# Optimization experiments

Hardware: AMD Instinct MI355X
Metric: run time of the kernel (lower is better)

Reference implementation:

```python
import jax, jax.numpy as jnp
import numpy as np

B, S, H, V = 2, 2048, 1024, 32000
SDS = [64, 128, 256]
EPS = 1e-5


def _ln(x, g, b):
    m = jnp.mean(x, -1, keepdims=True)
    v = jnp.var(x, -1, keepdims=True)
    return (x - m) * jax.lax.rsqrt(v + EPS) * g + b


def _layer(x, A_log, Wb, Wc, D, Wg, bg, Wo, bo, g, be):
    # x: [B,S,H]; state dim N = A_log.shape[0]
    A = jnp.exp(A_log)
    gate = jax.nn.sigmoid(jnp.einsum('bsh,nh->bsn', x, Wg) + bg)
    Bx = jnp.einsum('bsh,nh->bsn', x, Wb)
    u = gate * Bx  # [B,S,N]

    def step(s, u_t):
        s = A * s + u_t
        return s, s

    s0 = jnp.zeros((x.shape[0], A.shape[0]), x.dtype)
    _, states = jax.lax.scan(step, s0, jnp.swapaxes(u, 0, 1))  # [S,B,N]
    states = jnp.swapaxes(states, 0, 1)
    y = jnp.einsum('bsn,hn->bsh', states, Wc) + D * x
    out = _ln(y + x, g, be)
    return out @ Wo.T + bo  # dropout is identity (p used in eval / p=0)


def setup_inputs() -> dict:
    key = jax.random.key(0)
    ks = iter(jax.random.split(key, 64))
    d = {}
    d['x'] = jax.random.randint(next(ks), (B, S), 0, V)
    d['E'] = jax.random.normal(next(ks), (V, H), jnp.float32) * 0.02
    for i, N in enumerate(SDS):
        d[f'A{i}'] = jnp.log(jnp.exp(jnp.full((N,), -0.5)) + 0.1 * jax.random.normal(next(ks), (N,)))
        d[f'Wb{i}'] = jax.random.normal(next(ks), (N, H), jnp.float32) * 0.02
        d[f'Wc{i}'] = jax.random.normal(next(ks), (H, N), jnp.float32) * 0.02
        d[f'D{i}'] = jax.random.normal(next(ks), (H,), jnp.float32)
        d[f'Wg{i}'] = jax.random.normal(next(ks), (N, H), jnp.float32) * 0.02
        d[f'bg{i}'] = jnp.zeros((N,), jnp.float32)
        d[f'Wo{i}'] = jax.random.normal(next(ks), (H, H), jnp.float32) * 0.02
        d[f'bo{i}'] = jnp.zeros((H,), jnp.float32)
        d[f'g{i}'] = jnp.ones((H,), jnp.float32)
        d[f'be{i}'] = jnp.zeros((H,), jnp.float32)
    d['Wf'] = jax.random.normal(next(ks), (H, 3 * H), jnp.float32) * 0.02
    d['bf'] = jnp.zeros((H,), jnp.float32)
    d['gf'] = jnp.ones((H,), jnp.float32)
    d['bef'] = jnp.zeros((H,), jnp.float32)
    d['Wh'] = jax.random.normal(next(ks), (V, H), jnp.float32) * 0.02
    d['bh'] = jnp.zeros((V,), jnp.float32)
    return d


def reference(x, E,
              A0, Wb0, Wc0, D0, Wg0, bg0, Wo0, bo0, g0, be0,
              A1, Wb1, Wc1, D1, Wg1, bg1, Wo1, bo1, g1, be1,
              A2, Wb2, Wc2, D2, Wg2, bg2, Wo2, bo2, g2, be2,
              Wf, bf, gf, bef, Wh, bh):
    emb = E[x]  # [B,S,H]
    o0 = _layer(emb, A0, Wb0, Wc0, D0, Wg0, bg0, Wo0, bo0, g0, be0)
    o1 = _layer(emb, A1, Wb1, Wc1, D1, Wg1, bg1, Wo1, bo1, g1, be1)
    o2 = _layer(emb, A2, Wb2, Wc2, D2, Wg2, bg2, Wo2, bo2, g2, be2)
    combined = jnp.concatenate([o0, o1, o2], axis=-1)  # [B,S,3H]
    fused = combined @ Wf.T + bf
    fused = _ln(fused + emb, gf, bef)
    logits = fused @ Wh.T + bh  # [B,S,V]
    return logits
```

## Files before the change

kernel.cpp:

```cpp
#include <hip/hip_runtime.h>
#include <hip/hip_bf16.h>

#define Hd 1024
#define Bdim 2
#define Sd 2048
#define BSd 4096
#define Vd 32000
#define EPSf 1e-5f
#define CH 16
#define NCH 128
#define NT3 448

typedef __attribute__((ext_vector_type(8))) short short8;
typedef __attribute__((ext_vector_type(4))) float f32x4;
typedef __attribute__((ext_vector_type(4))) unsigned short us4;

__device__ __forceinline__ unsigned short f2bf(float f) {
  union { float f; unsigned int u; } v; v.f = f;
  return (unsigned short)((v.u + 0x7fffu + ((v.u >> 16) & 1u)) >> 16);
}

typedef __attribute__((address_space(1))) const void gvoid_t;
typedef __attribute__((address_space(3))) void svoid_t;
__device__ __forceinline__ void gl_lds16(const void* g, void* s) {
  __builtin_amdgcn_global_load_lds((gvoid_t*)g, (svoid_t*)s, 16, 0, 0);
}

struct CvtTab {
  const float* src[11];
  unsigned short* dst[11];
  int start[12];
};
__global__ void k_cvt_all(CvtTab tab) {
  int b = blockIdx.x;
  int j = 0;
  while (j < 10 && b >= tab.start[j + 1]) ++j;
  size_t i = (size_t)(b - tab.start[j]) * 256 + threadIdx.x;
  f32x4 v = *(const f32x4*)(tab.src[j] + i * 4);
  us4 o;
  o[0] = f2bf(v[0]); o[1] = f2bf(v[1]); o[2] = f2bf(v[2]); o[3] = f2bf(v[3]);
  *(us4*)(tab.dst[j] + i * 4) = o;
}

__global__ void k_cvtT(const float* __restrict__ s0, const float* __restrict__ s1,
                       const float* __restrict__ s2, unsigned short* __restrict__ dst) {
  const float* src = blockIdx.z == 0 ? s0 : (blockIdx.z == 1 ? s1 : s2);
  unsigned short* d = dst + (size_t)blockIdx.z * Hd * Hd;
  __shared__ float tile[32][33];
  int tx = threadIdx.x & 31, ty = threadIdx.x >> 5;
  int bx = blockIdx.x * 32, by = blockIdx.y * 32;
  #pragma unroll
  for (int i = 0; i < 4; ++i)
    tile[ty + i * 8][tx] = src[(size_t)(by + ty + i * 8) * Hd + bx + tx];
  __syncthreads();
  #pragma unroll
  for (int i = 0; i < 4; ++i)
    d[(size_t)(bx + ty + i * 8) * Hd + by + tx] = f2bf(tile[tx][ty + i * 8]);
}

__global__ void k_biasf(const float* __restrict__ Wf_, const float* __restrict__ bfb,
                        const float* __restrict__ bo0, const float* __restrict__ bo1,
                        const float* __restrict__ bo2, float* __restrict__ biasf) {
  int h = blockIdx.x, t = threadIdx.x;
  float s = 0.f;
  for (int c = t; c < 3072; c += 256) {
    float b = c < 1024 ? bo0[c] : (c < 2048 ? bo1[c - 1024] : bo2[c - 2048]);
    s += Wf_[(size_t)h * 3072 + c] * b;
  }
  #pragma unroll
  for (int o = 32; o >= 1; o >>= 1) s += __shfl_xor(s, o);
  __shared__ float red[4];
  if ((t & 63) == 0) red[t >> 6] = s;
  __syncthreads();
  if (t == 0) biasf[h] = bfb[h] + red[0] + red[1] + red[2] + red[3];
}

__global__ void k_setup(const float* A0, const float* A1, const float* A2,
                        const float* b0, const float* b1, const float* b2,
                        const float* D0, const float* D1, const float* D2,
                        const float* g0, const float* g1, const float* g2,
                        const float* e0, const float* e1, const float* e2,
                        float* Alog448, float* bg448,
                        float* D3, float* g3, float* be3) {
  int t = blockIdx.x * 256 + threadIdx.x;
  if (t < NT3) {
    int l = t < 64 ? 0 : (t < 192 ? 1 : 2);
    int o = t - (l == 0 ? 0 : (l == 1 ? 64 : 192));
    Alog448[t] = (l == 0 ? A0 : (l == 1 ? A1 : A2))[o];
    bg448[t]   = (l == 0 ? b0 : (l == 1 ? b1 : b2))[o];
  }
  if (t < 3072) {
    int l = t >> 10, o = t & 1023;
    D3[t]  = (l == 0 ? D0 : (l == 1 ? D1 : D2))[o];
    g3[t]  = (l == 0 ? g0 : (l == 1 ? g1 : g2))[o];
    be3[t] = (l == 0 ? e0 : (l == 1 ? e1 : e2))[o];
  }
}

__global__ void k_embed(const int* __restrict__ x, const float* __restrict__ E,
                        float* __restrict__ emb, unsigned short* __restrict__ embbf) {
  int row = blockIdx.x, t = threadIdx.x;
  int id = x[row];
  f32x4 v = *(const f32x4*)(E + (size_t)id * Hd + t * 4);
  *(f32x4*)(emb + (size_t)row * Hd + t * 4) = v;
  us4 o;
  o[0] = f2bf(v[0]); o[1] = f2bf(v[1]); o[2] = f2bf(v[2]); o[3] = f2bf(v[3]);
  *(us4*)(embbf + (size_t)row * Hd + t * 4) = o;
}

template<int BM, int BN, int WM, int WN, int BF16_OUT>
__launch_bounds__(WM * WN * 64)
__global__ void gemm2ph(const unsigned short* __restrict__ A,
                        const unsigned short* __restrict__ Bw,
                        const float* __restrict__ bias,
                        void* __restrict__ Cv,
                        int N, int K, int lda, int ldb, int ldc, int coff, int tm)
{
  constexpr int NT = WM * WN * 64;
  constexpr int MF = BM / WM / 16;
  constexpr int NF = BN / WN / 16;
  constexpr int ASZ = BM * 64;
  constexpr int BSZ = BN * 64;
  constexpr int AR = (ASZ * 2) / (NT * 16);
  constexpr int BR = (BSZ * 2) / (NT * 16);
  __shared__ __align__(16) unsigned short Sm[2 * (ASZ + BSZ)];

  int T = gridDim.x;
  int orig = blockIdx.x;
  int q = T >> 3, r = T & 7;
  int xc = orig & 7, sdv = orig >> 3;
  int wgid = (xc < r ? xc * (q + 1) : r * (q + 1) + (xc - r) * q) + sdv;
  int n_t = wgid / tm, m_t = wgid % tm;
  int row0 = m_t * BM, col0 = n_t * BN;

  int tid = threadIdx.x;
  int wave = tid >> 6, lane = tid & 63;
  int wm = wave / WN, wn = wave % WN;
  int wr = wm * (BM / WM), wc = wn * (BN / WN);
  int lr = lane & 15;
  int klane = lane >> 4;

  f32x4 acc[MF][NF] = {};

  auto stage = [&](int buf, int k0) {
    unsigned short* Ab = Sm + buf * (ASZ + BSZ);
    unsigned short* Bb = Ab + ASZ;
    #pragma unroll
    for (int j = 0; j < AR; ++j) {
      int slot = j * NT + tid;
      int lrow = slot >> 3, c16 = slot & 7;
      int scol = (c16 ^ (lrow & 7)) * 8;
      gl_lds16(A + (size_t)(row0 + lrow) * lda + k0 + scol, Ab + (j * NT + wave * 64) * 8);
    }
    #pragma unroll
    for (int j = 0; j < BR; ++j) {
      int slot = j * NT + tid;
      int lrow = slot >> 3, c16 = slot & 7;
      int scol = (c16 ^ (lrow & 7)) * 8;
      int brow = col0 + lrow;
      if (brow >= N) brow = N - 1;
      gl_lds16(Bw + (size_t)brow * ldb + k0 + scol, Bb + (j * NT + wave * 64) * 8);
    }
  };

  auto compute = [&](int buf) {
    const unsigned short* Ab = Sm + buf * (ASZ + BSZ);
    const unsigned short* Bb = Ab + ASZ;
    #pragma unroll
    for (int kk = 0; kk < 2; ++kk) {
      short8 afr[MF], bfr[NF];
      #pragma unroll
      for (int m = 0; m < MF; ++m) {
        int row = wr + m * 16 + lr;
        int cs = (kk * 4 + klane) ^ (row & 7);
        afr[m] = *(const short8*)(Ab + row * 64 + cs * 8);
      }
      #pragma unroll
      for (int n = 0; n < NF; ++n) {
        int row = wc + n * 16 + lr;
        int cs = (kk * 4 + klane) ^ (row & 7);
        bfr[n] = *(const short8*)(Bb + row * 64 + cs * 8);
      }
      #pragma unroll
      for (int m = 0; m < MF; ++m)
        #pragma unroll
        for (int n = 0; n < NF; ++n)
          acc[m][n] = __builtin_amdgcn_mfma_f32_16x16x32_bf16(afr[m], bfr[n], acc[m][n], 0, 0, 0);
    }
  };

  int nt = K >> 6;
  stage(0, 0);
  __syncthreads();
  for (int t = 0; t < nt - 1; ++t) {
    stage((t & 1) ^ 1, (t + 1) * 64);
    compute(t & 1);
    __syncthreads();
  }
  compute((nt - 1) & 1);

  int rb = (lane >> 4) * 4;
  #pragma unroll
  for (int m = 0; m < MF; ++m) {
    #pragma unroll
    for (int n = 0; n < NF; ++n) {
      int gcol = col0 + wc + n * 16 + lr;
      if (gcol >= N) continue;
      float bv = bias ? bias[gcol] : 0.f;
      #pragma unroll
      for (int j = 0; j < 4; ++j) {
        int grow = row0 + wr + m * 16 + rb + j;
        float val = acc[m][n][j] + bv;
        if (BF16_OUT)
          ((unsigned short*)Cv)[(size_t)grow * ldc + coff + gcol] = f2bf(val);
        else
          ((float*)Cv)[(size_t)grow * ldc + coff + gcol] = val;
      }
    }
  }
}

__launch_bounds__(256)
__global__ void gemm_wc3(const unsigned short* __restrict__ St,
                         const unsigned short* __restrict__ Wc,
                         float* __restrict__ Cv)
{
  constexpr int ASZ = 128 * 64, BSZ = 128 * 64;
  __shared__ __align__(16) unsigned short Sm[2 * (ASZ + BSZ)];
  int T = gridDim.x;
  int orig = blockIdx.x;
  int q = T >> 3, r = T & 7;
  int xc = orig & 7, sdv = orig >> 3;
  int wgid = (xc < r ? xc * (q + 1) : r * (q + 1) + (xc - r) * q) + sdv;
  int l = wgid % 3;
  int w2 = wgid / 3;
  int n_t = w2 >> 5, m_t = w2 & 31;
  const int owgl = l == 0 ? 0 : (l == 1 ? 64 : 192);
  const int K = 64 << l;
  const unsigned short* A = St + owgl;
  const unsigned short* Bw = Wc + (size_t)owgl * Hd;
  int row0 = m_t * 128, col0 = n_t * 128;

  int tid = threadIdx.x;
  int wave = tid >> 6, lane = tid & 63;
  int wm = wave >> 1, wn = wave & 1;
  int wr = wm * 64, wc = wn * 64;
  int lr = lane & 15, klane = lane >> 4;

  f32x4 acc[4][4] = {};
  auto stage = [&](int buf, int k0) {
    unsigned short* Ab = Sm + buf * (ASZ + BSZ);
    unsigned short* Bb = Ab + ASZ;
    #pragma unroll
    for (int j = 0; j < 4; ++j) {
      int slot = j * 256 + tid;
      int lrow = slot >> 3, c16 = slot & 7;
      int scol = (c16 ^ (lrow & 7)) * 8;
      gl_lds16(A + (size_t)(row0 + lrow) * NT3 + k0 + scol, Ab + (j * 256 + wave * 64) * 8);
      gl_lds16(Bw + (size_t)(col0 + lrow) * K + k0 + scol, Bb + (j * 256 + wave * 64) * 8);
    }
  };
  auto compute = [&](int buf) {
    const unsigned short* Ab = Sm + buf * (ASZ + BSZ);
    const unsigned short* Bb = Ab + ASZ;
    #pragma unroll
    for (int kk = 0; kk < 2; ++kk) {
      short8 afr[4], bfr[4];
      #pragma unroll
      for (int m = 0; m < 4; ++m) {
        int row = wr + m * 16 + lr;
        int cs = (kk * 4 + klane) ^ (row & 7);
        afr[m] = *(const short8*)(Ab + row * 64 + cs * 8);
      }
      #pragma unroll
      for (int n = 0; n < 4; ++n) {
        int row = wc + n * 16 + lr;
        int cs = (kk * 4 + klane) ^ (row & 7);
        bfr[n] = *(const short8*)(Bb + row * 64 + cs * 8);
      }
      #pragma unroll
      for (int m = 0; m < 4; ++m)
        #pragma unroll
        for (int n = 0; n < 4; ++n)
          acc[m][n] = __builtin_amdgcn_mfma_f32_16x16x32_bf16(afr[m], bfr[n], acc[m][n], 0, 0, 0);
    }
  };
  int nt = K >> 6;
  stage(0, 0);
  __syncthreads();
  for (int t = 0; t < nt - 1; ++t) {
    stage((t & 1) ^ 1, (t + 1) * 64);
    compute(t & 1);
    __syncthreads();
  }
  compute((nt - 1) & 1);

  int rb = (lane >> 4) * 4;
  #pragma unroll
  for (int m = 0; m < 4; ++m)
    #pragma unroll
    for (int n = 0; n < 4; ++n) {
      int gcol = l * Hd + col0 + wc + n * 16 + lr;
      #pragma unroll
      for (int j = 0; j < 4; ++j) {
        int grow = row0 + wr + m * 16 + rb + j;
        Cv[(size_t)grow * 3072 + gcol] = acc[m][n][j];
      }
    }
}

__launch_bounds__(256)
__global__ void gemm_bd3(const unsigned short* __restrict__ Awf,
                         const unsigned short* __restrict__ Bwo,
                         unsigned short* __restrict__ Cw)
{
  constexpr int ASZ = 128 * 64, BSZ = 128 * 64;
  __shared__ __align__(16) unsigned short Sm[2 * (ASZ + BSZ)];
  int T = gridDim.x;
  int orig = blockIdx.x;
  int q = T >> 3, r = T & 7;
  int xc = orig & 7, sdv = orig >> 3;
  int wgid = (xc < r ? xc * (q + 1) : r * (q + 1) + (xc - r) * q) + sdv;
  int n_g = wgid / 8, m_t = wgid % 8;
  int li = n_g >> 3, n_t = n_g & 7;
  const unsigned short* A = Awf + li * Hd;
  const unsigned short* Bw = Bwo + ((size_t)li << 20);
  int row0 = m_t * 128, col0 = n_t * 128;

  int tid = threadIdx.x;
  int wave = tid >> 6, lane = tid & 63;
  int wm = wave >> 1, wn = wave & 1;
  int wr = wm * 64, wc = wn * 64;
  int lr = lane & 15, klane = lane >> 4;

  f32x4 acc[4][4] = {};
  auto stage = [&](int buf, int k0) {
    unsigned short* Ab = Sm + buf * (ASZ + BSZ);
    unsigned short* Bb = Ab + ASZ;
    #pragma unroll
    for (int j = 0; j < 4; ++j) {
      int slot = j * 256 + tid;
      int lrow = slot >> 3, c16 = slot & 7;
      int scol = (c16 ^ (lrow & 7)) * 8;
      gl_lds16(A + (size_t)(row0 + lrow) * 3072 + k0 + scol, Ab + (j * 256 + wave * 64) * 8);
      gl_lds16(Bw + (size_t)(col0 + lrow) * 1024 + k0 + scol, Bb + (j * 256 + wave * 64) * 8);
    }
  };
  auto compute = [&](int buf) {
    const unsigned short* Ab = Sm + buf * (ASZ + BSZ);
    const unsigned short* Bb = Ab + ASZ;
    #pragma unroll
    for (int kk = 0; kk < 2; ++kk) {
      short8 afr[4], bfr[4];
      #pragma unroll
      for (int m = 0; m < 4; ++m) {
        int row = wr + m * 16 + lr;
        int cs = (kk * 4 + klane) ^ (row & 7);
        afr[m] = *(const short8*)(Ab + row * 64 + cs * 8);
      }
      #pragma unroll
      for (int n = 0; n < 4; ++n) {
        int row = wc + n * 16 + lr;
        int cs = (kk * 4 + klane) ^ (row & 7);
        bfr[n] = *(const short8*)(Bb + row * 64 + cs * 8);
      }
      #pragma unroll
      for (int m = 0; m < 4; ++m)
        #pragma unroll
        for (int n = 0; n < 4; ++n)
          acc[m][n] = __builtin_amdgcn_mfma_f32_16x16x32_bf16(afr[m], bfr[n], acc[m][n], 0, 0, 0);
    }
  };
  stage(0, 0);
  __syncthreads();
  for (int t = 0; t < 15; ++t) {
    stage((t & 1) ^ 1, (t + 1) * 64);
    compute(t & 1);
    __syncthreads();
  }
  compute(1);

  int rb = (lane >> 4) * 4;
  #pragma unroll
  for (int m = 0; m < 4; ++m)
    #pragma unroll
    for (int n = 0; n < 4; ++n) {
      int gcol = li * Hd + col0 + wc + n * 16 + lr;
      #pragma unroll
      for (int j = 0; j < 4; ++j) {
        int grow = row0 + wr + m * 16 + rb + j;
        Cw[(size_t)grow * 3072 + gcol] = f2bf(acc[m][n][j]);
      }
    }
}

__launch_bounds__(512)
__global__ void gemm8ph(const unsigned short* __restrict__ A,
                        const unsigned short* __restrict__ Bw,
                        const float* __restrict__ bias,
                        float* __restrict__ Cv,
                        int N, int K, int lda, int ldb, int ldc, int tn)
{
  __shared__ __align__(16) unsigned short Sm[65536];

  int wgid = blockIdx.x;
  int grp = wgid >> 8;
  int rem = wgid & 255;
  int n_t = grp * 16 + (rem >> 4);
  int m_t = rem & 15;
  int row0 = m_t * 256, col0 = n_t * 256;

  int tid = threadIdx.x;
  int wave = tid >> 6, lane = tid & 63;
  int wm = wave >> 2, wn = wave & 3;
  int lr = lane & 15, klane = lane >> 4;

  f32x4 acc[8][4] = {};

  auto stageA = [&](int b, int h, int kt) {
    unsigned short* base = Sm + (b * 2 + h) * 8192;
    #pragma unroll
    for (int j = 0; j < 2; ++j) {
      int slot = j * 512 + tid;
      int lrow = slot >> 3, c16 = slot & 7;
      int scol = (c16 ^ (lrow & 7)) * 8;
      gl_lds16(A + (size_t)(row0 + h * 128 + lrow) * lda + kt * 64 + scol,
               base + (j * 512 + wave * 64) * 8);
    }
  };
  auto stageB = [&](int b, int h, int kt) {
    unsigned short* base = Sm + 32768 + (b * 2 + h) * 8192;
    #pragma unroll
    for (int j = 0; j < 2; ++j) {
      int slot = j * 512 + tid;
      int lrow = slot >> 3, c16 = slot & 7;
      int scol = (c16 ^ (lrow & 7)) * 8;
      gl_lds16(Bw + (size_t)(col0 + h * 128 + lrow) * ldb + kt * 64 + scol,
               base + (j * 512 + wave * 64) * 8);
    }
  };
  auto readA = [&](short8* afr, int b, int mh, int kk) {
    const unsigned short* base = Sm + (b * 2 + mh) * 8192;
    #pragma unroll
    for (int f = 0; f < 4; ++f) {
      int rowin = f * 32 + wm * 16 + lr;
      int cs = (kk * 4 + klane) ^ (rowin & 7);
      afr[f] = *(const short8*)(base + rowin * 64 + cs * 8);
    }
  };
  auto readB = [&](short8* bfr, int b, int kk) {
    #pragma unroll
    for (int n = 0; n < 4; ++n) {
      int rowin = (n & 1) * 64 + wn * 16 + lr;
      const unsigned short* base = Sm + 32768 + (b * 2 + (n >> 1)) * 8192;
      int cs = (kk * 4 + klane) ^ (rowin & 7);
      bfr[n] = *(const short8*)(base + rowin * 64 + cs * 8);
    }
  };

  #define MFMA16(mh, afr, bfr)                                                  \
    __builtin_amdgcn_s_setprio(1);                                              \
    _Pragma("unroll")                                                           \
    for (int f = 0; f < 4; ++f)                                                 \
      _Pragma("unroll")                                                         \
      for (int n = 0; n < 4; ++n)                                               \
        acc[(mh) * 4 + f][n] = __builtin_amdgcn_mfma_f32_16x16x32_bf16(         \
            afr[f], bfr[n], acc[(mh) * 4 + f][n], 0, 0, 0);                     \
    __builtin_amdgcn_s_setprio(0);

  #define BAR()   __builtin_amdgcn_s_barrier()
  #define VM4()   asm volatile("s_waitcnt vmcnt(4)" ::: "memory")
  #define VM0()   asm volatile("s_waitcnt vmcnt(0)" ::: "memory")

  int nt = K >> 6;
  int iters = K >> 7;

  stageA(0, 0, 0); stageB(0, 0, 0); stageB(0, 1, 0); stageA(0, 1, 0);
  stageA(1, 0, 1); stageB(1, 0, 1);
  VM4(); BAR();

  short8 afr[4], bfr0[4], bfr1[4];
  for (int i = 0; i < iters; ++i) {
    int t1 = 2 * i + 1, t2 = 2 * i + 2, t3 = 2 * i + 3;
    bool last = (i == iters - 1);
    readA(afr, 0, 0, 0); readB(bfr0, 0, 0);
    stageB(1, 1, t1); stageA(1, 1, t1);
    MFMA16(0, afr, bfr0);
    BAR();
    readA(afr, 0, 0, 1); readB(bfr1, 0, 1);
    MFMA16(0, afr, bfr1);
    BAR();
    readA(afr, 0, 1, 0);
    if (t2 < nt) stageA(0, 0, t2);
    MFMA16(1, afr, bfr0);
    BAR();
    readA(afr, 0, 1, 1);
    if (t2 < nt) stageB(0, 0, t2);
    MFMA16(1, afr, bfr1);
    if (last) { VM0(); } else { VM4(); }
    BAR();
    readA(afr, 1, 0, 0); readB(bfr0, 1, 0);
    if (t2 < nt) { stageB(0, 1, t2); stageA(0, 1, t2); }
    MFMA16(0, afr, bfr0);
    BAR();
    readA(afr, 1, 0, 1); readB(bfr1, 1, 1);
    MFMA16(0, afr, bfr1);
    BAR();
    readA(afr, 1, 1, 0);
    if (t3 < nt) stageA(1, 0, t3);
    MFMA16(1, afr, bfr0);
    BAR();
    readA(afr, 1, 1, 1);
    if (t3 < nt) stageB(1, 0, t3);
    MFMA16(1, afr, bfr1);
    if (!last) { VM4(); }
    BAR();
  }

  int rb = (lane >> 4) * 4;
  #pragma unroll
  for (int idx = 0; idx < 8; ++idx) {
    int mh = idx >> 2, f = idx & 3;
    int growb = row0 + mh * 128 + f * 32 + wm * 16 + rb;
    #pragma unroll
    for (int n = 0; n < 4; ++n) {
      int gcol = col0 + (n & 1) * 64 + (n >> 1) * 128 + wn * 16 + lr;
      float bv = bias[gcol];
      #pragma unroll
      for (int j = 0; j < 4; ++j)
        Cv[(size_t)(growb + j) * ldc + gcol] = acc[idx][n][j] + bv;
    }
  }
  #undef MFMA16
  #undef BAR
  #undef VM4
  #undef VM0
}

__global__ void k_scanA(const float* __restrict__ gzbx, const float* __restrict__ Alog448,
                        const float* __restrict__ bg448,
                        float* __restrict__ st, float* __restrict__ carry) {
  int gid = blockIdx.x * 256 + threadIdx.x;
  if (gid >= Bdim * NCH * NT3) return;
  int n = gid % NT3;
  int c = (gid / NT3) % NCH;
  int b = gid / (NT3 * NCH);
  float a = expf(Alog448[n]);
  float bgv = bg448[n];
  float s = 0.f;
  size_t rbase = (size_t)b * Sd + (size_t)c * CH;
  for (int t = 0; t < CH; ++t) {
    size_t row = rbase + t;
    float gzv = gzbx[row * 896 + n];
    float bxv = gzbx[row * 896 + 448 + n];
    float gv = 1.f / (1.f + expf(-(gzv + bgv)));
    s = a * s + gv * bxv;
    st[row * NT3 + n] = s;
  }
  carry[((size_t)b * NCH + c) * NT3 + n] = s;
}

__global__ void k_scanB(const float* __restrict__ carry, const float* __restrict__ Alog448,
                        float* __restrict__ cin) {
  int i = blockIdx.x * 256 + threadIdx.x;
  if (i >= Bdim * NT3) return;
  int b = i / NT3, n = i % NT3;
  float aC = expf((float)CH * Alog448[n]);
  float s = 0.f;
  for (int c = 0; c < NCH; ++c) {
    cin[((size_t)b * NCH + c) * NT3 + n] = s;
    s = aC * s + carry[((size_t)b * NCH + c) * NT3 + n];
  }
}

__global__ void k_scanC(const float* __restrict__ st, const float* __restrict__ cin,
                        const float* __restrict__ Alog448, unsigned short* __restrict__ stbf) {
  size_t gid = (size_t)blockIdx.x * 256 + threadIdx.x;
  if (gid >= (size_t)BSd * NT3) return;
  int n = gid % NT3;
  int row = gid / NT3;
  int b = row / Sd, sg = row % Sd;
  int c = sg / CH, t = sg % CH;
  float cv = cin[((size_t)b * NCH + c) * NT3 + n];
  float val = st[gid] + expf((float)(t + 1) * Alog448[n]) * cv;
  stbf[gid] = f2bf(val);
}

__global__ void k_ln3(const float* __restrict__ y3, const float* __restrict__ emb,
                      const float* __restrict__ D3, const float* __restrict__ g3,
                      const float* __restrict__ be3, unsigned short* __restrict__ z3) {
  int row = blockIdx.x, ly = blockIdx.y, t = threadIdx.x;
  const float* y = y3 + (size_t)row * 3072 + ly * 1024;
  f32x4 yv = *(const f32x4*)(y + t * 4);
  f32x4 ev = *(const f32x4*)(emb + (size_t)row * Hd + t * 4);
  float vals[4];
  float sum = 0.f, sq = 0.f;
  #pragma unroll
  for (int j = 0; j < 4; ++j) {
    float coef = D3[ly * 1024 + t * 4 + j] + 1.f;
    float v = yv[j] + coef * ev[j];
    vals[j] = v; sum += v; sq += v * v;
  }
  #pragma unroll
  for (int o = 32; o >= 1; o >>= 1) {
    sum += __shfl_xor(sum, o);
    sq += __shfl_xor(sq, o);
  }
  __shared__ float red[2][4];
  int w = t >> 6, lane = t & 63;
  if (lane == 0) { red[0][w] = sum; red[1][w] = sq; }
  __syncthreads();
  sum = red[0][0] + red[0][1] + red[0][2] + red[0][3];
  sq  = red[1][0] + red[1][1] + red[1][2] + red[1][3];
  float mean = sum * (1.f / Hd);
  float var = sq * (1.f / Hd) - mean * mean;
  float rs = rsqrtf(var + EPSf);
  us4 o4;
  #pragma unroll
  for (int j = 0; j < 4; ++j) {
    float z = (vals[j] - mean) * rs * g3[ly * 1024 + t * 4 + j] + be3[ly * 1024 + t * 4 + j];
    o4[j] = f2bf(z);
  }
  *(us4*)(z3 + (size_t)row * 3072 + ly * 1024 + t * 4) = o4;
}

__global__ void k_ln(const float* __restrict__ y, const float* __restrict__ emb,
                     const float* __restrict__ g, const float* __restrict__ be,
                     unsigned short* __restrict__ out) {
  int row = blockIdx.x, t = threadIdx.x;
  f32x4 yv = *(const f32x4*)(y + (size_t)row * Hd + t * 4);
  f32x4 ev = *(const f32x4*)(emb + (size_t)row * Hd + t * 4);
  float vals[4];
  float sum = 0.f, sq = 0.f;
  #pragma unroll
  for (int j = 0; j < 4; ++j) {
    float v = yv[j] + ev[j];
    vals[j] = v; sum += v; sq += v * v;
  }
  #pragma unroll
  for (int o = 32; o >= 1; o >>= 1) {
    sum += __shfl_xor(sum, o);
    sq += __shfl_xor(sq, o);
  }
  __shared__ float red[2][4];
  int w = t >> 6, lane = t & 63;
  if (lane == 0) { red[0][w] = sum; red[1][w] = sq; }
  __syncthreads();
  sum = red[0][0] + red[0][1] + red[0][2] + red[0][3];
  sq  = red[1][0] + red[1][1] + red[1][2] + red[1][3];
  float mean = sum * (1.f / Hd);
  float var = sq * (1.f / Hd) - mean * mean;
  float rs = rsqrtf(var + EPSf);
  us4 o4;
  #pragma unroll
  for (int j = 0; j < 4; ++j) {
    float z = (vals[j] - mean) * rs * g[t * 4 + j] + be[t * 4 + j];
    o4[j] = f2bf(z);
  }
  *(us4*)(out + (size_t)row * Hd + t * 4) = o4;
}

extern "C" void kernel_launch(void* const* d_in, const int* in_sizes, int n_in,
                              void* d_out, int out_size, void* d_ws, size_t ws_size,
                              hipStream_t stream) {
  (void)in_sizes; (void)n_in; (void)out_size; (void)ws_size;
  const int* x = (const int*)d_in[0];
  const float* E = (const float*)d_in[1];
  const float* Wf_ = (const float*)d_in[32];
  const float* bfb = (const float*)d_in[33];
  const float* gfp = (const float*)d_in[34];
  const float* bef = (const float*)d_in[35];
  const float* Wh_ = (const float*)d_in[36];
  const float* bh = (const float*)d_in[37];

  char* wsb = (char*)d_ws;
  size_t off = 0;
  auto alloc = [&](size_t bytes) -> void* {
    void* p = wsb + off;
    off += (bytes + 255) & ~(size_t)255;
    return p;
  };
  float* emb             = (float*)alloc((size_t)BSd * Hd * 4);
  unsigned short* embbf  = (unsigned short*)alloc((size_t)BSd * Hd * 2);
  unsigned short* wgwbbf = (unsigned short*)alloc((size_t)896 * Hd * 2);
  unsigned short* wcbf   = (unsigned short*)alloc((size_t)NT3 * Hd * 2);
  unsigned short* wotbf  = (unsigned short*)alloc((size_t)3 * Hd * Hd * 2);
  unsigned short* wfbf   = (unsigned short*)alloc((size_t)3 * Hd * Hd * 2);
  unsigned short* wcombbf= (unsigned short*)alloc((size_t)Hd * 3 * Hd * 2);
  unsigned short* whbf   = (unsigned short*)alloc((size_t)Vd * Hd * 2);
  float* gzbx            = (float*)alloc((size_t)BSd * 896 * 4);
  float* stl             = (float*)alloc((size_t)BSd * NT3 * 4);
  unsigned short* stbf   = (unsigned short*)alloc((size_t)BSd * NT3 * 2);
  float* carry           = (float*)alloc((size_t)Bdim * NCH * NT3 * 4);
  float* cin             = (float*)alloc((size_t)Bdim * NCH * NT3 * 4);
  float* ybuf3           = (float*)alloc((size_t)BSd * 3072 * 4);
  unsigned short* zbf3   = (unsigned short*)alloc((size_t)BSd * 3072 * 2);
  unsigned short* zbf    = (unsigned short*)alloc((size_t)BSd * Hd * 2);
  float* Alog448         = (float*)alloc(NT3 * 4);
  float* bg448           = (float*)alloc(NT3 * 4);
  float* D3              = (float*)alloc(3072 * 4);
  float* g3              = (float*)alloc(3072 * 4);
  float* be3             = (float*)alloc(3072 * 4);
  float* biasf           = (float*)alloc(Hd * 4);

  k_embed<<<BSd, 256, 0, stream>>>(x, E, emb, embbf);

  {
    CvtTab tab;
    const int rowoff_g[3] = {0, 64, 192};
    int j = 0;
    int n4s[11];
    for (int i = 0; i < 3; ++i) { tab.src[j] = (const float*)d_in[2 + 10 * i + 4]; tab.dst[j] = wgwbbf + (size_t)rowoff_g[i] * Hd;         n4s[j] = (64 << i) * Hd / 4; ++j; }
    for (int i = 0; i < 3; ++i) { tab.src[j] = (const float*)d_in[2 + 10 * i + 1]; tab.dst[j] = wgwbbf + (size_t)(448 + rowoff_g[i]) * Hd;  n4s[j] = (64 << i) * Hd / 4; ++j; }
    for (int i = 0; i < 3; ++i) { tab.src[j] = (const float*)d_in[2 + 10 * i + 2]; tab.dst[j] = wcbf + (size_t)rowoff_g[i] * Hd;            n4s[j] = (64 << i) * Hd / 4; ++j; }
    tab.src[j] = Wf_; tab.dst[j] = wfbf; n4s[j] = 3 * Hd * Hd / 4; ++j;
    tab.src[j] = Wh_; tab.dst[j] = whbf; n4s[j] = Vd * Hd / 4; ++j;
    tab.start[0] = 0;
    for (int k = 0; k < 11; ++k) tab.start[k + 1] = tab.start[k] + (n4s[k] + 255) / 256;
    k_cvt_all<<<tab.start[11], 256, 0, stream>>>(tab);
  }

  k_cvtT<<<dim3(32, 32, 3), 256, 0, stream>>>(
      (const float*)d_in[8], (const float*)d_in[18], (const float*)d_in[28], wotbf);

  k_setup<<<12, 256, 0, stream>>>(
      (const float*)d_in[2], (const float*)d_in[12], (const float*)d_in[22],
      (const float*)d_in[7], (const float*)d_in[17], (const float*)d_in[27],
      (const float*)d_in[5], (const float*)d_in[15], (const float*)d_in[25],
      (const float*)d_in[10], (const float*)d_in[20], (const float*)d_in[30],
      (const float*)d_in[11], (const float*)d_in[21], (const float*)d_in[31],
      Alog448, bg448, D3, g3, be3);

  k_biasf<<<Hd, 256, 0, stream>>>(Wf_, bfb,
      (const float*)d_in[9], (const float*)d_in[19], (const float*)d_in[29], biasf);

  gemm_bd3<<<192, 256, 0, stream>>>(wfbf, wotbf, wcombbf);

  const int TM = BSd / 128;

  gemm2ph<128,128,2,2,0><<<(896 / 128) * TM, 256, 0, stream>>>(
      embbf, wgwbbf, nullptr, gzbx, 896, Hd, Hd, Hd, 896, 0, TM);

  {
    int totA = Bdim * NCH * NT3;
    k_scanA<<<(totA + 255) / 256, 256, 0, stream>>>(gzbx, Alog448, bg448, stl, carry);
    k_scanB<<<(Bdim * NT3 + 255) / 256, 256, 0, stream>>>(carry, Alog448, cin);
    size_t totC = (size_t)BSd * NT3;
    k_scanC<<<(int)((totC + 255) / 256), 256, 0, stream>>>(stl, cin, Alog448, stbf);
  }

  gemm_wc3<<<768, 256, 0, stream>>>(stbf, wcbf, ybuf3);

  k_ln3<<<dim3(BSd, 3), 256, 0, stream>>>(ybuf3, emb, D3, g3, be3, zbf3);

  gemm2ph<128,128,2,2,0><<<(Hd / 128) * TM, 256, 0, stream>>>(
      zbf3, wcombbf, biasf, ybuf3, Hd, 3 * Hd, 3 * Hd, 3 * Hd, Hd, 0, TM);
  k_ln<<<BSd, 256, 0, stream>>>(ybuf3, emb, gfp, bef, zbf);

  const int TN = Vd / 256;
  gemm8ph<<<(BSd / 256) * TN, 512, 0, stream>>>(
      zbf, whbf, bh, (float*)d_out, Vd, Hd, Hd, Hd, Vd, TN);
}
```

Before: 550.2 us.

## Replace 256x256 LM-head GEMM with 256x128 triple-buffered K=32 kernel

The vocab projection GEMM moves from a 256x256 tile with an 8-phase double-buffered K=64 pipeline to a 256x128 tile with a simple triple-buffered K=32 loop. Each of the 8 waves now owns a 64x64 output block with 16 accumulators instead of 32. LDS use drops from 128KB to 72KB, and launch_bounds(512,4) asks the compiler for fewer registers. This aims at higher occupancy and simpler scheduling, but it lowers arithmetic intensity and doubles A-tile reloads across N tiles.

```diff
diff --git a/kernel.cpp b/kernel.cpp
--- a/kernel.cpp
+++ b/kernel.cpp
@@ -394,146 +394,106 @@
     }
 }
 
-__launch_bounds__(512)
-__global__ void gemm8ph(const unsigned short* __restrict__ A,
+__launch_bounds__(512, 4)
+__global__ void gemm_v3(const unsigned short* __restrict__ A,
                         const unsigned short* __restrict__ Bw,
                         const float* __restrict__ bias,
                         float* __restrict__ Cv,
-                        int N, int K, int lda, int ldb, int ldc, int tn)
+                        int N, int K, int lda, int ldb, int ldc)
 {
-  __shared__ __align__(16) unsigned short Sm[65536];
+  constexpr int ASZ = 256 * 32;
+  constexpr int BSZ = 128 * 32;
+  __shared__ __align__(16) unsigned short Sm[3 * (ASZ + BSZ)];
 
   int wgid = blockIdx.x;
-  int grp = wgid >> 8;
-  int rem = wgid & 255;
-  int n_t = grp * 16 + (rem >> 4);
+  int g = wgid >> 8, rem = wgid & 255;
+  int n_t = g * 16 + (rem >> 4);
   int m_t = rem & 15;
-  int row0 = m_t * 256, col0 = n_t * 256;
+  int row0 = m_t * 256, col0 = n_t * 128;
 
   int tid = threadIdx.x;
   int wave = tid >> 6, lane = tid & 63;
-  int wm = wave >> 2, wn = wave & 3;
+  int wm = wave >> 1, wn = wave & 1;
+  int wr = wm * 64, wc = wn * 64;
   int lr = lane & 15, klane = lane >> 4;
 
-  f32x4 acc[8][4] = {};
-
-  auto stageA = [&](int b, int h, int kt) {
-    unsigned short* base = Sm + (b * 2 + h) * 8192;
+  f32x4 acc[4][4] = {};
+
+  auto stage = [&](int buf, int kt) {
+    unsigned short* Ab = Sm + buf * (ASZ + BSZ);
+    unsigned short* Bb = Ab + ASZ;
+    int k0 = kt * 32;
     #pragma unroll
     for (int j = 0; j < 2; ++j) {
       int slot = j * 512 + tid;
-      int lrow = slot >> 3, c16 = slot & 7;
-      int scol = (c16 ^ (lrow & 7)) * 8;
-      gl_lds16(A + (size_t)(row0 + h * 128 + lrow) * lda + kt * 64 + scol,
-               base + (j * 512 + wave * 64) * 8);
+      int lrow = slot >> 2, c4 = slot & 3;
+      int scol = (c4 ^ ((lrow >> 1) & 3)) * 8;
+      gl_lds16(A + (size_t)(row0 + lrow) * lda + k0 + scol,
+               Ab + (j * 512 + wave * 64) * 8);
+    }
+    {
+      int lrow = tid >> 2, c4 = tid & 3;
+      int scol = (c4 ^ ((lrow >> 1) & 3)) * 8;
+      gl_lds16(Bw + (size_t)(col0 + lrow) * ldb + k0 + scol,
+               Bb + (wave * 64) * 8);
     }
   };
-  auto stageB = [&](int b, int h, int kt) {
-    unsigned short* base = Sm + 32768 + (b * 2 + h) * 8192;
-    #pragma unroll
-    for (int j = 0; j < 2; ++j) {
-      int slot = j * 512 + tid;
-      int lrow = slot >> 3, c16 = slot & 7;
-      int scol = (c16 ^ (lrow & 7)) * 8;
-      gl_lds16(Bw + (size_t)(col0 + h * 128 + lrow) * ldb + kt * 64 + scol,
-               base + (j * 512 + wave * 64) * 8);
-    }
-  };
-  auto readA = [&](short8* afr, int b, int mh, int kk) {
-    const unsigned short* base = Sm + (b * 2 + mh) * 8192;
-    #pragma unroll
-    for (int f = 0; f < 4; ++f) {
-      int rowin = f * 32 + wm * 16 + lr;
-      int cs = (kk * 4 + klane) ^ (rowin & 7);
-      afr[f] = *(const short8*)(base + rowin * 64 + cs * 8);
-    }
-  };
-  auto readB = [&](short8* bfr, int b, int kk) {
+
+  #define VM3()  asm volatile("s_waitcnt vmcnt(3)" ::: "memory")
+  #define VM0()  asm volatile("s_waitcnt vmcnt(0)" ::: "memory")
+
+  int nt = K >> 5;
+  stage(0, 0); stage(1, 1);
+  VM3();
+  __builtin_amdgcn_s_barrier();
+
+  int cb = 0, sb = 2;
+  for (int t = 0; t < nt; ++t) {
+    const unsigned short* Ab = Sm + cb * (ASZ + BSZ);
+    const unsigned short* Bb = Ab + ASZ;
+    short8 afr[4], bfr[4];
+    #pragma unroll
+    for (int m = 0; m < 4; ++m) {
+      int row = wr + m * 16 + lr;
+      int cs = klane ^ ((row >> 1) & 3);
+      afr[m] = *(const short8*)(Ab + row * 32 + cs * 8);
+    }
     #pragma unroll
     for (int n = 0; n < 4; ++n) {
-      int rowin = (n & 1) * 64 + wn * 16 + lr;
-      const unsigned short* base = Sm + 32768 + (b * 2 + (n >> 1)) * 8192;
-      int cs = (kk * 4 + klane) ^ (rowin & 7);
-      bfr[n] = *(const short8*)(base + rowin * 64 + cs * 8);
-    }
-  };
-
-  #define MFMA16(mh, afr, bfr)                                                  \
-    __builtin_amdgcn_s_setprio(1);                                              \
-    _Pragma("unroll")                                                           \
-    for (int f = 0; f < 4; ++f)                                                 \
-      _Pragma("unroll")                                                         \
-      for (int n = 0; n < 4; ++n)                                               \
-        acc[(mh) * 4 + f][n] = __builtin_amdgcn_mfma_f32_16x16x32_bf16(         \
-            afr[f], bfr[n], acc[(mh) * 4 + f][n], 0, 0, 0);                     \
+      int row = wc + n * 16 + lr;
+      int cs = klane ^ ((row >> 1) & 3);
+      bfr[n] = *(const short8*)(Bb + row * 32 + cs * 8);
+    }
+    if (t + 2 < nt) stage(sb, t + 2);
+    __builtin_amdgcn_s_setprio(1);
+    #pragma unroll
+    for (int m = 0; m < 4; ++m)
+      #pragma unroll
+      for (int n = 0; n < 4; ++n)
+        acc[m][n] = __builtin_amdgcn_mfma_f32_16x16x32_bf16(afr[m], bfr[n], acc[m][n], 0, 0, 0);
     __builtin_amdgcn_s_setprio(0);
-
-  #define BAR()   __builtin_amdgcn_s_barrier()
-  #define VM4()   asm volatile("s_waitcnt vmcnt(4)" ::: "memory")
-  #define VM0()   asm volatile("s_waitcnt vmcnt(0)" ::: "memory")
-
-  int nt = K >> 6;
-  int iters = K >> 7;
-
-  stageA(0, 0, 0); stageB(0, 0, 0); stageB(0, 1, 0); stageA(0, 1, 0);
-  stageA(1, 0, 1); stageB(1, 0, 1);
-  VM4(); BAR();
-
-  short8 afr[4], bfr0[4], bfr1[4];
-  for (int i = 0; i < iters; ++i) {
-    int t1 = 2 * i + 1, t2 = 2 * i + 2, t3 = 2 * i + 3;
-    bool last = (i == iters - 1);
-    readA(afr, 0, 0, 0); readB(bfr0, 0, 0);
-    stageB(1, 1, t1); stageA(1, 1, t1);
-    MFMA16(0, afr, bfr0);
-    BAR();
-    readA(afr, 0, 0, 1); readB(bfr1, 0, 1);
-    MFMA16(0, afr, bfr1);
-    BAR();
-    readA(afr, 0, 1, 0);
-    if (t2 < nt) stageA(0, 0, t2);
-    MFMA16(1, afr, bfr0);
-    BAR();
-    readA(afr, 0, 1, 1);
-    if (t2 < nt) stageB(0, 0, t2);
-    MFMA16(1, afr, bfr1);
-    if (last) { VM0(); } else { VM4(); }
-    BAR();
-    readA(afr, 1, 0, 0); readB(bfr0, 1, 0);
-    if (t2 < nt) { stageB(0, 1, t2); stageA(0, 1, t2); }
-    MFMA16(0, afr, bfr0);
-    BAR();
-    readA(afr, 1, 0, 1); readB(bfr1, 1, 1);
-    MFMA16(0, afr, bfr1);
-    BAR();
-    readA(afr, 1, 1, 0);
-    if (t3 < nt) stageA(1, 0, t3);
-    MFMA16(1, afr, bfr0);
-    BAR();
-    readA(afr, 1, 1, 1);
-    if (t3 < nt) stageB(1, 0, t3);
-    MFMA16(1, afr, bfr1);
-    if (!last) { VM4(); }
-    BAR();
-  }
-
-  int rb = (lane >> 4) * 4;
-  #pragma unroll
-  for (int idx = 0; idx < 8; ++idx) {
-    int mh = idx >> 2, f = idx & 3;
-    int growb = row0 + mh * 128 + f * 32 + wm * 16 + rb;
+    if (t < nt - 2)       { VM3(); }
+    else if (t == nt - 2) { VM0(); }
+    __builtin_amdgcn_s_barrier();
+    cb = (cb + 1 == 3) ? 0 : cb + 1;
+    sb = (sb + 1 == 3) ? 0 : sb + 1;
+  }
+
+  int rb = klane * 4;
+  #pragma unroll
+  for (int m = 0; m < 4; ++m) {
     #pragma unroll
     for (int n = 0; n < 4; ++n) {
-      int gcol = col0 + (n & 1) * 64 + (n >> 1) * 128 + wn * 16 + lr;
+      int gcol = col0 + wc + n * 16 + lr;
       float bv = bias[gcol];
       #pragma unroll
-      for (int j = 0; j < 4; ++j)
-        Cv[(size_t)(growb + j) * ldc + gcol] = acc[idx][n][j] + bv;
-    }
-  }
-  #undef MFMA16
-  #undef BAR
-  #undef VM4
+      for (int j = 0; j < 4; ++j) {
+        int grow = row0 + wr + m * 16 + rb + j;
+        Cv[(size_t)grow * ldc + gcol] = acc[m][n][j] + bv;
+      }
+    }
+  }
+  #undef VM3
   #undef VM0
 }
 
@@ -757,7 +717,6 @@
       zbf3, wcombbf, biasf, ybuf3, Hd, 3 * Hd, 3 * Hd, 3 * Hd, Hd, 0, TM);
   k_ln<<<BSd, 256, 0, stream>>>(ybuf3, emb, gfp, bef, zbf);
 
-  const int TN = Vd / 256;
-  gemm8ph<<<(BSd / 256) * TN, 512, 0, stream>>>(
-      zbf, whbf, bh, (float*)d_out, Vd, Hd, Hd, Hd, Vd, TN);
-}
+  gemm_v3<<<(BSd / 256) * (Vd / 128), 512, 0, stream>>>(
+      zbf, whbf, bh, (float*)d_out, Vd, Hd, Hd, Hd, Vd);
+}
```

Result: slower. 573.1 us (+4.2%).
